# Performance work log

Measured on AMD Instinct MI355X. Metric: run time of the kernel, lower is better.

## Reference

```python
import jax, jax.numpy as jnp
import numpy as np

N = 10000      # nodes
E = 160000     # edges
D_IN = 512
D_H = 512
P_DROP = 0.2


def _glorot(key, shape):
    lim = float(np.sqrt(6.0 / (shape[0] + shape[1])))
    return jax.random.uniform(key, shape, jnp.float32, -lim, lim)


def setup_inputs() -> dict:
    key = jax.random.key(0)
    ks = jax.random.split(key, 8)
    h = jax.random.normal(ks[0], (N, D_IN), jnp.float32)
    src = jax.random.randint(ks[1], (E,), 0, N)
    dst = jax.random.randint(ks[2], (E,), 0, N)
    edge_weight = jax.random.uniform(ks[3], (E,), jnp.float32)
    W0 = _glorot(ks[4], (D_IN, D_H))
    W1 = _glorot(ks[5], (D_H, D_H))
    W2 = _glorot(ks[6], (D_H, D_H))
    b0 = jnp.zeros((D_H,), jnp.float32)
    b1 = jnp.zeros((D_H,), jnp.float32)
    b2 = jnp.zeros((D_H,), jnp.float32)
    return dict(h=h, src=src, dst=dst, edge_weight=edge_weight,
                W0=W0, b0=b0, W1=W1, b1=b1, W2=W2, b2=b2)


def _dropout(x, key):
    keep = jax.random.bernoulli(key, 1.0 - P_DROP, x.shape)
    return jnp.where(keep, x / (1.0 - P_DROP), 0.0)


def _graph_conv(x, src, dst, ew, W, b, act):
    # DGL GraphConv, norm='both', weight=True, bias=True, with edge_weight.
    ones = jnp.ones((src.shape[0],), x.dtype)
    deg_out = jnp.maximum(jax.ops.segment_sum(ones, src, num_segments=N), 1.0)
    deg_in = jnp.maximum(jax.ops.segment_sum(ones, dst, num_segments=N), 1.0)
    x = x * (deg_out ** -0.5)[:, None]          # src norm
    msg = x[src] * ew[:, None]                  # [E, D] gather + edge weight
    agg = jax.ops.segment_sum(msg, dst, num_segments=N)  # scatter-add
    out = (agg @ W) * (deg_in ** -0.5)[:, None] + b
    return act(out) if act is not None else out


def reference(h, src, dst, edge_weight, W0, b0, W1, b1, W2, b2):
    dk = jax.random.split(jax.random.key(42), 3)
    x = _dropout(h, dk[0])
    x = _graph_conv(x, src, dst, edge_weight, W0, b0, jax.nn.elu)
    x = _dropout(x, dk[1])
    x = _graph_conv(x, src, dst, edge_weight, W1, b1, jax.nn.elu)
    x = _dropout(x, dk[2])
    x = _graph_conv(x, src, dst, edge_weight, W2, b2, None)
    return x
```

## Files before the change

kernel.cpp:

```cpp
#include <hip/hip_runtime.h>
#include <stdint.h>

#define N_NODES 10000
#define N_EDGES 160000
#define D 512
#define TOT (N_NODES * D)
#define M_PAD 10112
#define NMASK (TOT / 32)

typedef _Float16 h8 __attribute__((ext_vector_type(8)));
typedef _Float16 h2 __attribute__((ext_vector_type(2)));
typedef float f4 __attribute__((ext_vector_type(4)));

__host__ __device__ inline uint32_t rotl32(uint32_t v, int r) {
    return (v << r) | (v >> (32 - r));
}

__host__ __device__ inline void tf2x32(uint32_t k0, uint32_t k1,
                                       uint32_t& x0, uint32_t& x1) {
    uint32_t k2 = k0 ^ k1 ^ 0x1BD11BDAu;
    x0 += k0; x1 += k1;
    x0 += x1; x1 = rotl32(x1, 13); x1 ^= x0;
    x0 += x1; x1 = rotl32(x1, 15); x1 ^= x0;
    x0 += x1; x1 = rotl32(x1, 26); x1 ^= x0;
    x0 += x1; x1 = rotl32(x1,  6); x1 ^= x0;
    x0 += k1; x1 += k2 + 1u;
    x0 += x1; x1 = rotl32(x1, 17); x1 ^= x0;
    x0 += x1; x1 = rotl32(x1, 29); x1 ^= x0;
    x0 += x1; x1 = rotl32(x1, 16); x1 ^= x0;
    x0 += x1; x1 = rotl32(x1, 24); x1 ^= x0;
    x0 += k2; x1 += k0 + 2u;
    x0 += x1; x1 = rotl32(x1, 13); x1 ^= x0;
    x0 += x1; x1 = rotl32(x1, 15); x1 ^= x0;
    x0 += x1; x1 = rotl32(x1, 26); x1 ^= x0;
    x0 += x1; x1 = rotl32(x1,  6); x1 ^= x0;
    x0 += k0; x1 += k1 + 3u;
    x0 += x1; x1 = rotl32(x1, 17); x1 ^= x0;
    x0 += x1; x1 = rotl32(x1, 29); x1 ^= x0;
    x0 += x1; x1 = rotl32(x1, 16); x1 ^= x0;
    x0 += x1; x1 = rotl32(x1, 24); x1 ^= x0;
    x0 += k1; x1 += k2 + 4u;
    x0 += x1; x1 = rotl32(x1, 13); x1 ^= x0;
    x0 += x1; x1 = rotl32(x1, 15); x1 ^= x0;
    x0 += x1; x1 = rotl32(x1, 26); x1 ^= x0;
    x0 += x1; x1 = rotl32(x1,  6); x1 ^= x0;
    x0 += k2; x1 += k0 + 5u;
}

__device__ __forceinline__ uint32_t dropout_bit(uint32_t k0, uint32_t k1, uint32_t j) {
    uint32_t c0 = 0u, c1 = j;
    tf2x32(k0, k1, c0, c1);
    uint32_t bits = c0 ^ c1;
    float u = __uint_as_float((bits >> 9) | 0x3f800000u) - 1.0f;
    return (u < 0.8f) ? 1u : 0u;
}

#define HIST_BLKS 625
#define WCONV_BLKS 192
#define PRE_BLKS (HIST_BLKS + WCONV_BLKS + 5000)
__global__ __launch_bounds__(256)
void pre_kernel(const int* __restrict__ src, const int* __restrict__ dst,
                int* __restrict__ deg_out, int* __restrict__ deg_in,
                const float* __restrict__ W0, const float* __restrict__ W1,
                const float* __restrict__ W2, _Float16* __restrict__ Wt,
                const float* __restrict__ x, _Float16* __restrict__ y,
                uint32_t k0, uint32_t k1) {
    __shared__ float tile[64][65];
    int b = blockIdx.x;
    int t = threadIdx.x;
    if (b < HIST_BLKS) {
        int e = b * 256 + t;
        if (e < N_EDGES) {
            atomicAdd(&deg_out[src[e]], 1);
            atomicAdd(&deg_in[dst[e]], 1);
        }
    } else if (b < HIST_BLKS + WCONV_BLKS) {
        int b2 = b - HIST_BLKS;
        int bx = b2 & 7, by = (b2 >> 3) & 7, bz = b2 >> 6;
        const float* W = (bz == 0) ? W0 : (bz == 1) ? W1 : W2;
        _Float16* T = Wt + (size_t)bz * 512 * 512;
        int r0 = by * 64, c0 = bx * 64;
        int c = t & 63, rq = t >> 6;
#pragma unroll
        for (int i = 0; i < 16; ++i) {
            int r = rq + i * 4;
            tile[r][c] = W[(size_t)(r0 + r) * 512 + c0 + c];
        }
        __syncthreads();
        int k = t & 63, nq = t >> 6;
#pragma unroll
        for (int i = 0; i < 16; ++i) {
            int n = nq + i * 4;
            T[(size_t)(c0 + n) * 512 + r0 + k] = (_Float16)tile[k][n];
        }
    } else {
        int b3 = b - HIST_BLKS - WCONV_BLKS;
        int j = (b3 * 256 + t) * 4;
        if (j >= TOT) return;
        float4 xv = *(const float4*)&x[j];
        _Float16 r[4];
        uint32_t jj = (uint32_t)j;
#pragma unroll
        for (int i = 0; i < 4; ++i) {
            float g = dropout_bit(k0, k1, jj + (uint32_t)i) ? 1.0f : 0.0f;
            float xi = (&xv.x)[i];
            r[i] = (_Float16)(g * (xi / 0.8f));
        }
        *(ushort4*)&y[j] = *(ushort4*)r;
    }
}

__global__ __launch_bounds__(1024)
void scan_kernel(const int* __restrict__ deg_in, const int* __restrict__ deg_out,
                 int* __restrict__ row_ptr,
                 float* __restrict__ rn_in, float* __restrict__ rn_out) {
    __shared__ int wsum[16];
    int tid = threadIdx.x;
    int lane = tid & 63, wv = tid >> 6;
    int base = tid * 10;
    int v[10];
    int tot = 0;
#pragma unroll
    for (int i = 0; i < 10; ++i) {
        int idx = base + i;
        v[i] = (idx < N_NODES) ? deg_in[idx] : 0;
        tot += v[i];
    }
    int s = tot;
#pragma unroll
    for (int off = 1; off < 64; off <<= 1) {
        int t = __shfl_up(s, off, 64);
        if (lane >= off) s += t;
    }
    if (lane == 63) wsum[wv] = s;
    __syncthreads();
    if (wv == 0 && lane < 16) {
        int ws = wsum[lane];
#pragma unroll
        for (int off = 1; off < 16; off <<= 1) {
            int t = __shfl_up(ws, off, 64);
            if (lane >= off) ws += t;
        }
        wsum[lane] = ws;
    }
    __syncthreads();
    int run = ((wv > 0) ? wsum[wv - 1] : 0) + (s - tot);
#pragma unroll
    for (int i = 0; i < 10; ++i) {
        int idx = base + i;
        if (idx < N_NODES) {
            row_ptr[idx] = run;
            rn_in[idx]  = 1.0f / sqrtf(fmaxf((float)v[i], 1.0f));
            rn_out[idx] = 1.0f / sqrtf(fmaxf((float)deg_out[idx], 1.0f));
        }
        run += v[i];
    }
    if (tid == 1023) row_ptr[N_NODES] = wsum[15];
}

__global__ void fill_kernel(const int* __restrict__ src, const int* __restrict__ dst,
                            const float* __restrict__ ew, const int* __restrict__ row_ptr,
                            const float* __restrict__ rn_out,
                            int* __restrict__ cursor, int2* __restrict__ csr) {
    int e = blockIdx.x * 256 + threadIdx.x;
    if (e >= N_EDGES) return;
    int v = dst[e];
    int sn = src[e];
    int pos = atomicAdd(&cursor[v], 1);
    int idx = row_ptr[v] + pos;
    csr[idx] = make_int2(sn, __float_as_int(ew[e] * rn_out[sn]));
}

__global__ __launch_bounds__(256)
void aggregate_kernel(const _Float16* __restrict__ y, const int* __restrict__ row_ptr,
                      const int2* __restrict__ csr, _Float16* __restrict__ agg,
                      uint32_t* __restrict__ mask, uint32_t mk0, uint32_t mk1) {
    int node = blockIdx.x * 4 + (threadIdx.x >> 6);
    int lane = threadIdx.x & 63;
    int cs = blockIdx.y;
    const _Float16* ys = y + cs * 128 + lane * 2;
    int beg = row_ptr[node], end = row_ptr[node + 1];
    float a0 = 0.f, a1 = 0.f;
    int k = beg;
    for (; k + 7 < end; k += 8) {
        int2 e[8];
#pragma unroll
        for (int i = 0; i < 8; ++i) e[i] = csr[k + i];
        h2 v[8];
#pragma unroll
        for (int i = 0; i < 8; ++i) v[i] = *(const h2*)&ys[(size_t)e[i].x * 512];
#pragma unroll
        for (int i = 0; i < 8; ++i) {
            float w = __int_as_float(e[i].y);
            a0 += w * (float)v[i][0];
            a1 += w * (float)v[i][1];
        }
    }
    for (; k < end; ++k) {
        int2 e0 = csr[k];
        float w = __int_as_float(e0.y);
        h2 v = *(const h2*)&ys[(size_t)e0.x * 512];
        a0 += w * (float)v[0];
        a1 += w * (float)v[1];
    }
    h2 r;
    r[0] = (_Float16)a0;
    r[1] = (_Float16)a1;
    *(h2*)&agg[(size_t)node * 512 + cs * 128 + lane * 2] = r;

    if (cs == 0 && mask) {
        int gtid = blockIdx.x * 256 + threadIdx.x;
        if (gtid < NMASK) {
            uint32_t w = 0, jb = (uint32_t)gtid * 32u;
#pragma unroll 4
            for (int i = 0; i < 32; ++i)
                w |= dropout_bit(mk0, mk1, jb + (uint32_t)i) << i;
            mask[gtid] = w;
        }
    }
}

#define GBK 32
#define LDA 40
__global__ __launch_bounds__(256)
void gemm_kernel(const _Float16* __restrict__ A, const _Float16* __restrict__ Wt,
                 const float* __restrict__ bias, const float* __restrict__ rn_in,
                 _Float16* __restrict__ yout, float* __restrict__ fout,
                 int mode, const uint32_t* __restrict__ mask) {
    __shared__ _Float16 As[128 * LDA];
    __shared__ _Float16 Bs[128 * LDA];
    int tid = threadIdx.x;
    int wv = tid >> 6, lane = tid & 63;

    int f = blockIdx.x + blockIdx.y * 4;
    int xcd = f & 7, jj = f >> 3;
    int T = ((xcd < 4) ? xcd * 40 : 160 + (xcd - 4) * 39) + jj;
    int row0 = (T >> 2) * 128, col0 = (T & 3) * 128;

    int wr = wv >> 1, wc = wv & 1;

    f4 acc[4][4];
#pragma unroll
    for (int i = 0; i < 4; ++i)
#pragma unroll
        for (int j = 0; j < 4; ++j) acc[i][j] = (f4){0.f, 0.f, 0.f, 0.f};

    int srow = tid >> 2;
    int sseg = (tid & 3) * 8;
    const _Float16* gA0 = A + (size_t)(row0 + srow) * 512 + sseg;
    const _Float16* gA1 = gA0 + (size_t)64 * 512;
    const _Float16* gB0 = Wt + (size_t)(col0 + srow) * 512 + sseg;
    const _Float16* gB1 = gB0 + (size_t)64 * 512;
    _Float16* wA0 = &As[srow * LDA + sseg];
    _Float16* wA1 = &As[(64 + srow) * LDA + sseg];
    _Float16* wB0 = &Bs[srow * LDA + sseg];
    _Float16* wB1 = &Bs[(64 + srow) * LDA + sseg];

    int kf = (lane >> 4) * 8;
    const _Float16* fa = &As[(wr * 64 + (lane & 15)) * LDA + kf];
    const _Float16* fb = &Bs[(wc * 64 + (lane & 15)) * LDA + kf];

    h8 ra0 = *(const h8*)gA0;
    h8 ra1 = *(const h8*)gA1;
    h8 rb0 = *(const h8*)gB0;
    h8 rb1 = *(const h8*)gB1;

    for (int kk = 0; kk < 512; kk += GBK) {
        *(h8*)wA0 = ra0;
        *(h8*)wA1 = ra1;
        *(h8*)wB0 = rb0;
        *(h8*)wB1 = rb1;
        __syncthreads();
        if (kk + GBK < 512) {
            ra0 = *(const h8*)(gA0 + kk + GBK);
            ra1 = *(const h8*)(gA1 + kk + GBK);
            rb0 = *(const h8*)(gB0 + kk + GBK);
            rb1 = *(const h8*)(gB1 + kk + GBK);
        }
        h8 af[4], bf[4];
#pragma unroll
        for (int mt = 0; mt < 4; ++mt) af[mt] = *(const h8*)(fa + mt * 16 * LDA);
#pragma unroll
        for (int nt = 0; nt < 4; ++nt) bf[nt] = *(const h8*)(fb + nt * 16 * LDA);
#pragma unroll
        for (int mt = 0; mt < 4; ++mt)
#pragma unroll
            for (int nt = 0; nt < 4; ++nt)
                acc[mt][nt] = __builtin_amdgcn_mfma_f32_16x16x32_f16(
                    af[mt], bf[nt], acc[mt][nt], 0, 0, 0);
        __syncthreads();
    }

    int mbase = row0 + wr * 64;
    int nbase = col0 + wc * 64;
#pragma unroll
    for (int mt = 0; mt < 4; ++mt) {
#pragma unroll
        for (int nt = 0; nt < 4; ++nt) {
            int gr0 = mbase + mt * 16 + (lane >> 4) * 4;
            int gc = nbase + nt * 16 + (lane & 15);
            float bcol = bias[gc];
#pragma unroll
            for (int i = 0; i < 4; ++i) {
                int gr = gr0 + i;
                if (gr >= N_NODES) continue;
                float v = acc[mt][nt][i] * rn_in[gr] + bcol;
                if (mode == 0) {
                    v = (v > 0.f) ? v : expm1f(v);
                    uint32_t j = (uint32_t)(gr * 512 + gc);
                    uint32_t g = (mask[j >> 5] >> (j & 31)) & 1u;
                    v = g ? (v / 0.8f) : 0.0f;
                    yout[(size_t)gr * 512 + gc] = (_Float16)v;
                } else {
                    fout[(size_t)gr * 512 + gc] = v;
                }
            }
        }
    }
}

extern "C" void kernel_launch(void* const* d_in, const int* in_sizes, int n_in,
                              void* d_out, int out_size, void* d_ws, size_t ws_size,
                              hipStream_t stream) {
    const float* h   = (const float*)d_in[0];
    const int*   src = (const int*)d_in[1];
    const int*   dst = (const int*)d_in[2];
    const float* ew  = (const float*)d_in[3];
    const float* W0  = (const float*)d_in[4];
    const float* b0  = (const float*)d_in[5];
    const float* W1  = (const float*)d_in[6];
    const float* b1  = (const float*)d_in[7];
    const float* W2  = (const float*)d_in[8];
    const float* b2  = (const float*)d_in[9];
    const float* bl[3] = {b0, b1, b2};
    float* out = (float*)d_out;

    char* ws = (char*)d_ws;
    _Float16* y16  = (_Float16*)ws; ws += (size_t)TOT * 2;
    _Float16* aggF = (_Float16*)ws; ws += (size_t)M_PAD * 512 * 2;
    _Float16* Wt   = (_Float16*)ws; ws += (size_t)3 * 512 * 512 * 2;
    int* degi_in  = (int*)ws;  ws += N_NODES * 4;
    int* degi_out = (int*)ws;  ws += N_NODES * 4;
    int* cursor   = (int*)ws;  ws += N_NODES * 4;
    int* row_ptr  = (int*)ws;  ws += (N_NODES + 1) * 4;
    ws = (char*)(((uintptr_t)ws + 15) & ~(uintptr_t)15);
    int2* csr     = (int2*)ws; ws += (size_t)N_EDGES * 8;
    float* rn_in  = (float*)ws; ws += N_NODES * 4;
    float* rn_out = (float*)ws; ws += N_NODES * 4;
    uint32_t* maskbuf = (uint32_t*)ws; ws += (size_t)NMASK * 4;

    hipMemsetAsync(degi_in, 0, 3 * N_NODES * 4, stream);

    uint32_t dk[3][2];
    for (int i = 0; i < 3; ++i) {
        uint32_t c0 = 0u, c1 = (uint32_t)i;
        tf2x32(0u, 42u, c0, c1);
        dk[i][0] = c0; dk[i][1] = c1;
    }

    pre_kernel<<<PRE_BLKS, 256, 0, stream>>>(src, dst, degi_out, degi_in,
                                             W0, W1, W2, Wt, h, y16,
                                             dk[0][0], dk[0][1]);
    scan_kernel<<<1, 1024, 0, stream>>>(degi_in, degi_out, row_ptr, rn_in, rn_out);
    fill_kernel<<<(N_EDGES + 255) / 256, 256, 0, stream>>>(src, dst, ew, row_ptr,
                                                           rn_out, cursor, csr);

    for (int l = 0; l < 3; ++l) {
        uint32_t* mk = (l < 2) ? maskbuf : nullptr;
        uint32_t mk0 = (l < 2) ? dk[l + 1][0] : 0u;
        uint32_t mk1 = (l < 2) ? dk[l + 1][1] : 0u;
        aggregate_kernel<<<dim3(N_NODES / 4, 4), 256, 0, stream>>>(
            y16, row_ptr, csr, aggF, mk, mk0, mk1);
        int mode = (l < 2) ? 0 : 1;
        gemm_kernel<<<dim3(4, M_PAD / 128), 256, 0, stream>>>(
            aggF, Wt + (size_t)l * 512 * 512, bl[l], rn_in,
            y16, out, mode, maskbuf);
    }
}
```

Before: 360.8 us.

## Shrink GEMM tiles to 64x64 with 128-deep K chunks and remap blocks

The GEMM tile goes from 128x128 with K-step 32 to 64x64 with K-step 128, and the launch grows from 316 to 1264 blocks on a 1D grid with an XCD-aware tile mapping. Smaller tiles give more blocks to spread over the CUs, and deeper K chunks cut the number of sync barriers to four per tile. The cost is less operand reuse per block, so there is more global and LDS traffic per FLOP, and fewer MFMAs per wave between barriers.

```diff
diff --git a/kernel.cpp b/kernel.cpp
--- a/kernel.cpp
+++ b/kernel.cpp
@@ -220,83 +220,81 @@
     }
 }
 
-#define GBK 32
-#define LDA 40
+#define GBK 128
+#define LDA2 136
 __global__ __launch_bounds__(256)
 void gemm_kernel(const _Float16* __restrict__ A, const _Float16* __restrict__ Wt,
                  const float* __restrict__ bias, const float* __restrict__ rn_in,
                  _Float16* __restrict__ yout, float* __restrict__ fout,
                  int mode, const uint32_t* __restrict__ mask) {
-    __shared__ _Float16 As[128 * LDA];
-    __shared__ _Float16 Bs[128 * LDA];
+    __shared__ _Float16 As[64 * LDA2];
+    __shared__ _Float16 Bs[64 * LDA2];
     int tid = threadIdx.x;
     int wv = tid >> 6, lane = tid & 63;
 
-    int f = blockIdx.x + blockIdx.y * 4;
-    int xcd = f & 7, jj = f >> 3;
-    int T = ((xcd < 4) ? xcd * 40 : 160 + (xcd - 4) * 39) + jj;
-    int row0 = (T >> 2) * 128, col0 = (T & 3) * 128;
+    int f = blockIdx.x;
+    int T = (f & 7) * 158 + (f >> 3);
+    int row0 = (T >> 3) * 64, col0 = (T & 7) * 64;
 
     int wr = wv >> 1, wc = wv & 1;
 
-    f4 acc[4][4];
-#pragma unroll
-    for (int i = 0; i < 4; ++i)
-#pragma unroll
-        for (int j = 0; j < 4; ++j) acc[i][j] = (f4){0.f, 0.f, 0.f, 0.f};
-
-    int srow = tid >> 2;
-    int sseg = (tid & 3) * 8;
-    const _Float16* gA0 = A + (size_t)(row0 + srow) * 512 + sseg;
-    const _Float16* gA1 = gA0 + (size_t)64 * 512;
-    const _Float16* gB0 = Wt + (size_t)(col0 + srow) * 512 + sseg;
-    const _Float16* gB1 = gB0 + (size_t)64 * 512;
-    _Float16* wA0 = &As[srow * LDA + sseg];
-    _Float16* wA1 = &As[(64 + srow) * LDA + sseg];
-    _Float16* wB0 = &Bs[srow * LDA + sseg];
-    _Float16* wB1 = &Bs[(64 + srow) * LDA + sseg];
-
-    int kf = (lane >> 4) * 8;
-    const _Float16* fa = &As[(wr * 64 + (lane & 15)) * LDA + kf];
-    const _Float16* fb = &Bs[(wc * 64 + (lane & 15)) * LDA + kf];
-
-    h8 ra0 = *(const h8*)gA0;
-    h8 ra1 = *(const h8*)gA1;
-    h8 rb0 = *(const h8*)gB0;
-    h8 rb1 = *(const h8*)gB1;
+    f4 acc[2][2];
+#pragma unroll
+    for (int i = 0; i < 2; ++i)
+#pragma unroll
+        for (int j = 0; j < 2; ++j) acc[i][j] = (f4){0.f, 0.f, 0.f, 0.f};
+
+    int r = tid >> 2;
+    int cseg = (tid & 3) * 32;
+    const _Float16* gA = A  + (size_t)(row0 + r) * 512 + cseg;
+    const _Float16* gB = Wt + (size_t)(col0 + r) * 512 + cseg;
+    _Float16* wA = &As[r * LDA2 + cseg];
+    _Float16* wB = &Bs[r * LDA2 + cseg];
+
+    const _Float16* fa = &As[(wr * 32 + (lane & 15)) * LDA2 + (lane >> 4) * 8];
+    const _Float16* fb = &Bs[(wc * 32 + (lane & 15)) * LDA2 + (lane >> 4) * 8];
+
+    h8 ra[4], rb[4];
+#pragma unroll
+    for (int i = 0; i < 4; ++i) {
+        ra[i] = *(const h8*)(gA + i * 8);
+        rb[i] = *(const h8*)(gB + i * 8);
+    }
 
     for (int kk = 0; kk < 512; kk += GBK) {
-        *(h8*)wA0 = ra0;
-        *(h8*)wA1 = ra1;
-        *(h8*)wB0 = rb0;
-        *(h8*)wB1 = rb1;
+#pragma unroll
+        for (int i = 0; i < 4; ++i) {
+            *(h8*)(wA + i * 8) = ra[i];
+            *(h8*)(wB + i * 8) = rb[i];
+        }
         __syncthreads();
         if (kk + GBK < 512) {
-            ra0 = *(const h8*)(gA0 + kk + GBK);
-            ra1 = *(const h8*)(gA1 + kk + GBK);
-            rb0 = *(const h8*)(gB0 + kk + GBK);
-            rb1 = *(const h8*)(gB1 + kk + GBK);
-        }
-        h8 af[4], bf[4];
-#pragma unroll
-        for (int mt = 0; mt < 4; ++mt) af[mt] = *(const h8*)(fa + mt * 16 * LDA);
-#pragma unroll
-        for (int nt = 0; nt < 4; ++nt) bf[nt] = *(const h8*)(fb + nt * 16 * LDA);
-#pragma unroll
-        for (int mt = 0; mt < 4; ++mt)
-#pragma unroll
-            for (int nt = 0; nt < 4; ++nt)
-                acc[mt][nt] = __builtin_amdgcn_mfma_f32_16x16x32_f16(
-                    af[mt], bf[nt], acc[mt][nt], 0, 0, 0);
+#pragma unroll
+            for (int i = 0; i < 4; ++i) {
+                ra[i] = *(const h8*)(gA + kk + GBK + i * 8);
+                rb[i] = *(const h8*)(gB + kk + GBK + i * 8);
+            }
+        }
+#pragma unroll
+        for (int s = 0; s < 4; ++s) {
+            h8 af0 = *(const h8*)(fa + s * 32);
+            h8 af1 = *(const h8*)(fa + 16 * LDA2 + s * 32);
+            h8 bf0 = *(const h8*)(fb + s * 32);
+            h8 bf1 = *(const h8*)(fb + 16 * LDA2 + s * 32);
+            acc[0][0] = __builtin_amdgcn_mfma_f32_16x16x32_f16(af0, bf0, acc[0][0], 0, 0, 0);
+            acc[0][1] = __builtin_amdgcn_mfma_f32_16x16x32_f16(af0, bf1, acc[0][1], 0, 0, 0);
+            acc[1][0] = __builtin_amdgcn_mfma_f32_16x16x32_f16(af1, bf0, acc[1][0], 0, 0, 0);
+            acc[1][1] = __builtin_amdgcn_mfma_f32_16x16x32_f16(af1, bf1, acc[1][1], 0, 0, 0);
+        }
         __syncthreads();
     }
 
-    int mbase = row0 + wr * 64;
-    int nbase = col0 + wc * 64;
-#pragma unroll
-    for (int mt = 0; mt < 4; ++mt) {
-#pragma unroll
-        for (int nt = 0; nt < 4; ++nt) {
+    int mbase = row0 + wr * 32;
+    int nbase = col0 + wc * 32;
+#pragma unroll
+    for (int mt = 0; mt < 2; ++mt) {
+#pragma unroll
+        for (int nt = 0; nt < 2; ++nt) {
             int gr0 = mbase + mt * 16 + (lane >> 4) * 4;
             int gc = nbase + nt * 16 + (lane & 15);
             float bcol = bias[gc];
@@ -372,7 +370,7 @@
         aggregate_kernel<<<dim3(N_NODES / 4, 4), 256, 0, stream>>>(
             y16, row_ptr, csr, aggF, mk, mk0, mk1);
         int mode = (l < 2) ? 0 : 1;
-        gemm_kernel<<<dim3(4, M_PAD / 128), 256, 0, stream>>>(
+        gemm_kernel<<<1264, 256, 0, stream>>>(
             aggF, Wt + (size_t)l * 512 * 512, bl[l], rn_in,
             y16, out, mode, maskbuf);
     }
```

New measurement: 329.5 us. 8.7% less time.
